# Kernel optimization log

Hardware: AMD Instinct MI355X
Metric: run time of the kernel (lower is better)

Reference implementation:

```python
import jax, jax.numpy as jnp
import numpy as np

B = 4096
UNITS = 2048
INP = 2048


def setup_inputs() -> dict:
    key = jax.random.key(0)
    k1, k2, k3, k4 = jax.random.split(key, 4)
    pre_layer = jax.random.normal(k1, (2, B, UNITS), dtype=jnp.float32)
    x = jax.random.normal(k2, (B, INP), dtype=jnp.float32)
    W = jax.random.normal(k3, (4, UNITS, INP), dtype=jnp.float32) * 0.02
    U = jax.random.normal(k4, (4, UNITS, UNITS), dtype=jnp.float32) * 0.02
    return {"pre_layer": pre_layer, "x": x, "W": W, "U": U}


def reference(pre_layer, x, W, U):
    pre_h, pre_c = pre_layer[0], pre_layer[1]
    # Fuse the 8 matmuls into 2 batched GEMMs: gates[g] = x @ W[g].T + pre_h @ U[g].T
    gates = jnp.einsum('bi,gui->gbu', x, W) + jnp.einsum('bh,guh->gbu', pre_h, U)
    i_t = jax.nn.sigmoid(gates[0])
    f_t = jax.nn.sigmoid(gates[1])
    o_t = jax.nn.sigmoid(gates[2])
    n_c_t = jnp.tanh(gates[3])
    c = f_t * pre_c + i_t * n_c_t
    h = o_t * jnp.tanh(c)
    return jnp.stack([h, c])
```

## Files before the change

kernel.cpp:

```cpp
#include <hip/hip_runtime.h>
#include <hip/hip_bf16.h>

#define B_DIM 4096
#define UNITS_DIM 2048
#define K_DIM 4096
#define M_DIM 8192

typedef __bf16 bf16x8 __attribute__((ext_vector_type(8)));
typedef float f32x4 __attribute__((ext_vector_type(4)));

#define AS1C(p) ((const __attribute__((address_space(1))) void*)(p))
#define AS3(p)  ((__attribute__((address_space(3))) void*)(p))

__device__ __forceinline__ float fast_sigmoid(float x) {
    return 1.0f / (1.0f + __expf(-x));
}
__device__ __forceinline__ float fast_tanh(float x) {
    return 2.0f / (1.0f + __expf(-2.0f * x)) - 1.0f;
}

__global__ void convert_act(const float* __restrict__ pre_h,
                            const float* __restrict__ x,
                            __hip_bfloat16* __restrict__ Abf) {
    const long long idx = (long long)blockIdx.x * blockDim.x + threadIdx.x;
    const long long e = idx * 8;
    const int b = (int)(e >> 12);
    const int k = (int)(e & 4095);
    const float* src = (k < UNITS_DIM)
        ? (x + (long long)b * UNITS_DIM + k)
        : (pre_h + (long long)b * UNITS_DIM + (k - UNITS_DIM));
    float4 f0 = ((const float4*)src)[0];
    float4 f1 = ((const float4*)src)[1];
    union { __hip_bfloat16 h[8]; uint4 u4; } p;
    p.h[0] = __float2bfloat16(f0.x); p.h[1] = __float2bfloat16(f0.y);
    p.h[2] = __float2bfloat16(f0.z); p.h[3] = __float2bfloat16(f0.w);
    p.h[4] = __float2bfloat16(f1.x); p.h[5] = __float2bfloat16(f1.y);
    p.h[6] = __float2bfloat16(f1.z); p.h[7] = __float2bfloat16(f1.w);
    *(uint4*)(Abf + e) = p.u4;
}

__global__ void convert_wu(const float* __restrict__ W,
                           const float* __restrict__ U,
                           __hip_bfloat16* __restrict__ Bbf) {
    const long long idx = (long long)blockIdx.x * blockDim.x + threadIdx.x;
    const long long e = idx * 8;
    const int n = (int)(e >> 12);
    const int k = (int)(e & 4095);
    const int u = n >> 2;
    const int g = n & 3;
    const float* src = (k < UNITS_DIM)
        ? (W + ((long long)g * UNITS_DIM + u) * UNITS_DIM + k)
        : (U + ((long long)g * UNITS_DIM + u) * UNITS_DIM + (k - UNITS_DIM));
    float4 f0 = ((const float4*)src)[0];
    float4 f1 = ((const float4*)src)[1];
    union { __hip_bfloat16 h[8]; uint4 u4; } p;
    p.h[0] = __float2bfloat16(f0.x); p.h[1] = __float2bfloat16(f0.y);
    p.h[2] = __float2bfloat16(f0.z); p.h[3] = __float2bfloat16(f0.w);
    p.h[4] = __float2bfloat16(f1.x); p.h[5] = __float2bfloat16(f1.y);
    p.h[6] = __float2bfloat16(f1.z); p.h[7] = __float2bfloat16(f1.w);
    *(uint4*)(Bbf + e) = p.u4;
}

__global__ __launch_bounds__(512, 2) void lstm_gemm(
    const __hip_bfloat16* __restrict__ Wc,
    const __hip_bfloat16* __restrict__ Ac,
    const float* __restrict__ pre_c,
    float* __restrict__ out)
{
    __shared__ __hip_bfloat16 As[4 * 8192];
    __shared__ __hip_bfloat16 Bs[4 * 8192];

    const int tid  = threadIdx.x;
    const int lane = tid & 63;
    const int wave = tid >> 6;

    const int bid  = blockIdx.x;
    const int wgid = (bid & 7) * 64 + (bid >> 3);
    const int m_base = (wgid & 31) * 256;
    const int n_base = (wgid >> 5) * 256;

    const int wm  = (wave >> 2) * 128;
    const int wn  = (wave & 3) * 64;
    const int l15 = lane & 15;
    const int lq  = lane >> 4;
    const int keyr = (l15 >> 1) & 3;

    const int aofs = (wm + l15) * 32 + ((lq ^ keyr) * 8);
    const int bofs = (wn + l15) * 32 + ((lq ^ keyr) * 8);

    const int r0 = tid >> 2;
    const int gc = (((tid & 3) ^ ((tid >> 3) & 3)) * 8);
    const __hip_bfloat16* wg0 = Wc + (size_t)(m_base + r0) * K_DIM + gc;
    const __hip_bfloat16* ag0 = Ac + (size_t)(n_base + r0) * K_DIM + gc;

#define STAGE(T) do {                                                          \
        const int sb_ = (T) & 3;                                               \
        const size_t ko_ = (size_t)(T) * 32;                                   \
        __builtin_amdgcn_global_load_lds(AS1C(wg0 + ko_),                      \
            AS3(As + sb_ * 8192 + tid * 8), 16, 0, 0);                         \
        __builtin_amdgcn_global_load_lds(AS1C(wg0 + (size_t)128 * K_DIM + ko_),\
            AS3(As + sb_ * 8192 + 4096 + tid * 8), 16, 0, 0);                  \
        __builtin_amdgcn_global_load_lds(AS1C(ag0 + ko_),                      \
            AS3(Bs + sb_ * 8192 + tid * 8), 16, 0, 0);                         \
        __builtin_amdgcn_global_load_lds(AS1C(ag0 + (size_t)128 * K_DIM + ko_),\
            AS3(Bs + sb_ * 8192 + 4096 + tid * 8), 16, 0, 0);                  \
    } while (0)

    f32x4 acc[8][4] = {};

    STAGE(0);
    STAGE(1);
    STAGE(2);
    asm volatile("s_waitcnt vmcnt(8)" ::: "memory");
    __builtin_amdgcn_s_barrier();

    for (int t = 0; t < 128; ++t) {
        const int buf = t & 3;
        const __hip_bfloat16* Ab = As + buf * 8192 + aofs;
        const __hip_bfloat16* Bb = Bs + buf * 8192 + bofs;
        bf16x8 af[8], bfv[4];
#pragma unroll
        for (int mi = 0; mi < 8; ++mi)
            af[mi] = *(const bf16x8*)(Ab + mi * 512);
#pragma unroll
        for (int ni = 0; ni < 4; ++ni)
            bfv[ni] = *(const bf16x8*)(Bb + ni * 512);

        if (t < 125) STAGE(t + 3);

        __builtin_amdgcn_sched_barrier(0);
        asm volatile("s_waitcnt lgkmcnt(0)" ::: "memory");
        if (t < 125)
            asm volatile("s_waitcnt vmcnt(8)" ::: "memory");
        else if (t == 125)
            asm volatile("s_waitcnt vmcnt(4)" ::: "memory");
        else
            asm volatile("s_waitcnt vmcnt(0)" ::: "memory");
        __builtin_amdgcn_s_barrier();
        __builtin_amdgcn_sched_barrier(0);

        __builtin_amdgcn_s_setprio(1);
#pragma unroll
        for (int mi = 0; mi < 8; ++mi)
#pragma unroll
            for (int ni = 0; ni < 4; ++ni)
                acc[mi][ni] = __builtin_amdgcn_mfma_f32_16x16x32_bf16(
                    af[mi], bfv[ni], acc[mi][ni], 0, 0, 0);
        __builtin_amdgcn_s_setprio(0);
    }
#undef STAGE

#pragma unroll
    for (int mi = 0; mi < 8; ++mi) {
        const int u = ((m_base + wm + mi * 16) >> 2) + lq;
#pragma unroll
        for (int ni = 0; ni < 4; ++ni) {
            const int b = n_base + wn + ni * 16 + l15;
            f32x4 gv = acc[mi][ni];
            float i_t = fast_sigmoid(gv[0]);
            float f_t = fast_sigmoid(gv[1]);
            float o_t = fast_sigmoid(gv[2]);
            float n_t = fast_tanh(gv[3]);
            float pc  = pre_c[(size_t)b * UNITS_DIM + u];
            float c   = f_t * pc + i_t * n_t;
            float h   = o_t * fast_tanh(c);
            out[(size_t)b * UNITS_DIM + u] = h;
            out[(size_t)B_DIM * UNITS_DIM + (size_t)b * UNITS_DIM + u] = c;
        }
    }
}

extern "C" void kernel_launch(void* const* d_in, const int* in_sizes, int n_in,
                              void* d_out, int out_size, void* d_ws, size_t ws_size,
                              hipStream_t stream) {
    const float* pre_layer = (const float*)d_in[0];
    const float* x         = (const float*)d_in[1];
    const float* W         = (const float*)d_in[2];
    const float* U         = (const float*)d_in[3];
    float* out = (float*)d_out;

    const float* pre_h = pre_layer;
    const float* pre_c = pre_layer + (size_t)B_DIM * UNITS_DIM;

    __hip_bfloat16* Abf = (__hip_bfloat16*)d_ws;
    __hip_bfloat16* Bbf = (__hip_bfloat16*)((char*)d_ws +
                          (size_t)B_DIM * K_DIM * sizeof(__hip_bfloat16));

    convert_act<<<8192, 256, 0, stream>>>(pre_h, x, Abf);
    convert_wu<<<16384, 256, 0, stream>>>(W, U, Bbf);

    lstm_gemm<<<512, 512, 0, stream>>>(Bbf, Abf, pre_c, out);
}
```

Measured before the change: 505.2 us.

## Restructure GEMM main loop into four-phase ping-pong schedule with split stages

Replaces the 4-deep single-phase k-loop with a double-buffered 64-wide k-step split into four sub-phases. Each phase loads half the A fragments, issues one A or B half-stage of global-to-LDS loads, then runs 16 MFMAs between barriers. The aim is to interleave LDS reads, global prefetch and MFMA work more finely and reduce register pressure for fragments. In exchange it adds more barriers per k-step and a tighter vmcnt accounting that must match the issue order.

Measured after the change: 642.4 us. +27.2%, slower.

```diff
diff --git a/kernel.cpp b/kernel.cpp
--- a/kernel.cpp
+++ b/kernel.cpp
@@ -67,8 +67,8 @@
     const float* __restrict__ pre_c,
     float* __restrict__ out)
 {
-    __shared__ __hip_bfloat16 As[4 * 8192];
-    __shared__ __hip_bfloat16 Bs[4 * 8192];
+    __shared__ __hip_bfloat16 As[32768];
+    __shared__ __hip_bfloat16 Bs[32768];
 
     const int tid  = threadIdx.x;
     const int lane = tid & 63;
@@ -83,72 +83,122 @@
     const int wn  = (wave & 3) * 64;
     const int l15 = lane & 15;
     const int lq  = lane >> 4;
-    const int keyr = (l15 >> 1) & 3;
-
-    const int aofs = (wm + l15) * 32 + ((lq ^ keyr) * 8);
-    const int bofs = (wn + l15) * 32 + ((lq ^ keyr) * 8);
-
-    const int r0 = tid >> 2;
+    const int key = (l15 >> 1) & 3;
+
+    const int aro = (wm + l15) * 32 + ((lq ^ key) * 8);
+    const int bro = (wn + l15) * 32 + ((lq ^ key) * 8);
+
     const int gc = (((tid & 3) ^ ((tid >> 3) & 3)) * 8);
-    const __hip_bfloat16* wg0 = Wc + (size_t)(m_base + r0) * K_DIM + gc;
-    const __hip_bfloat16* ag0 = Ac + (size_t)(n_base + r0) * K_DIM + gc;
-
-#define STAGE(T) do {                                                          \
-        const int sb_ = (T) & 3;                                               \
-        const size_t ko_ = (size_t)(T) * 32;                                   \
+    const __hip_bfloat16* wg0 = Wc + (size_t)(m_base + (tid >> 2)) * K_DIM + gc;
+    const __hip_bfloat16* ag0 = Ac + (size_t)(n_base + (tid >> 2)) * K_DIM + gc;
+
+#define STAGE_A(T, KK) do {                                                    \
+        const int b_ = ((T) & 1) * 16384 + (KK) * 8192;                        \
+        const size_t ko_ = (size_t)(T) * 64 + (KK) * 32;                       \
         __builtin_amdgcn_global_load_lds(AS1C(wg0 + ko_),                      \
-            AS3(As + sb_ * 8192 + tid * 8), 16, 0, 0);                         \
+            AS3(As + b_ + tid * 8), 16, 0, 0);                                 \
         __builtin_amdgcn_global_load_lds(AS1C(wg0 + (size_t)128 * K_DIM + ko_),\
-            AS3(As + sb_ * 8192 + 4096 + tid * 8), 16, 0, 0);                  \
+            AS3(As + b_ + 4096 + tid * 8), 16, 0, 0);                          \
+    } while (0)
+#define STAGE_B(T, KK) do {                                                    \
+        const int b_ = ((T) & 1) * 16384 + (KK) * 8192;                        \
+        const size_t ko_ = (size_t)(T) * 64 + (KK) * 32;                       \
         __builtin_amdgcn_global_load_lds(AS1C(ag0 + ko_),                      \
-            AS3(Bs + sb_ * 8192 + tid * 8), 16, 0, 0);                         \
+            AS3(Bs + b_ + tid * 8), 16, 0, 0);                                 \
         __builtin_amdgcn_global_load_lds(AS1C(ag0 + (size_t)128 * K_DIM + ko_),\
-            AS3(Bs + sb_ * 8192 + 4096 + tid * 8), 16, 0, 0);                  \
+            AS3(Bs + b_ + 4096 + tid * 8), 16, 0, 0);                          \
     } while (0)
 
+#define PHASE_SYNC() do {                                                      \
+        __builtin_amdgcn_s_barrier();                                          \
+        asm volatile("s_waitcnt lgkmcnt(0)" ::: "memory");                     \
+        __builtin_amdgcn_sched_barrier(0);                                     \
+    } while (0)
+
     f32x4 acc[8][4] = {};
 
-    STAGE(0);
-    STAGE(1);
-    STAGE(2);
-    asm volatile("s_waitcnt vmcnt(8)" ::: "memory");
+    STAGE_B(0, 0); STAGE_A(0, 0); STAGE_B(0, 1); STAGE_A(0, 1);
+    STAGE_B(1, 0); STAGE_A(1, 0); STAGE_B(1, 1);
+    asm volatile("s_waitcnt vmcnt(6)" ::: "memory");
     __builtin_amdgcn_s_barrier();
 
-    for (int t = 0; t < 128; ++t) {
-        const int buf = t & 3;
-        const __hip_bfloat16* Ab = As + buf * 8192 + aofs;
-        const __hip_bfloat16* Bb = Bs + buf * 8192 + bofs;
-        bf16x8 af[8], bfv[4];
-#pragma unroll
-        for (int mi = 0; mi < 8; ++mi)
-            af[mi] = *(const bf16x8*)(Ab + mi * 512);
+    for (int k = 0; k < 64; ++k) {
+        const int buf = (k & 1) * 16384;
+        const __hip_bfloat16* Ab = As + buf + aro;
+        const __hip_bfloat16* Bb = Bs + buf + bro;
+        bf16x8 af[4], bfv[4];
+
+#pragma unroll
+        for (int mi = 0; mi < 4; ++mi) af[mi] = *(const bf16x8*)(Ab + mi * 512);
+#pragma unroll
+        for (int ni = 0; ni < 4; ++ni) bfv[ni] = *(const bf16x8*)(Bb + ni * 512);
+        if (k <= 62) STAGE_A(k + 1, 1);
+        PHASE_SYNC();
+        __builtin_amdgcn_s_setprio(1);
+#pragma unroll
+        for (int mi = 0; mi < 4; ++mi)
+#pragma unroll
+            for (int ni = 0; ni < 4; ++ni)
+                acc[mi][ni] = __builtin_amdgcn_mfma_f32_16x16x32_bf16(
+                    af[mi], bfv[ni], acc[mi][ni], 0, 0, 0);
+        __builtin_amdgcn_s_setprio(0);
+        __builtin_amdgcn_s_barrier();
+
+#pragma unroll
+        for (int mi = 0; mi < 4; ++mi)
+            af[mi] = *(const bf16x8*)(Ab + (4 + mi) * 512);
+        if (k <= 61) STAGE_B(k + 2, 0);
+        PHASE_SYNC();
+        __builtin_amdgcn_s_setprio(1);
+#pragma unroll
+        for (int mi = 0; mi < 4; ++mi)
+#pragma unroll
+            for (int ni = 0; ni < 4; ++ni)
+                acc[4 + mi][ni] = __builtin_amdgcn_mfma_f32_16x16x32_bf16(
+                    af[mi], bfv[ni], acc[4 + mi][ni], 0, 0, 0);
+        __builtin_amdgcn_s_setprio(0);
+        __builtin_amdgcn_s_barrier();
+
+#pragma unroll
+        for (int mi = 0; mi < 4; ++mi)
+            af[mi] = *(const bf16x8*)(Ab + 8192 + mi * 512);
 #pragma unroll
         for (int ni = 0; ni < 4; ++ni)
-            bfv[ni] = *(const bf16x8*)(Bb + ni * 512);
-
-        if (t < 125) STAGE(t + 3);
-
-        __builtin_amdgcn_sched_barrier(0);
-        asm volatile("s_waitcnt lgkmcnt(0)" ::: "memory");
-        if (t < 125)
-            asm volatile("s_waitcnt vmcnt(8)" ::: "memory");
-        else if (t == 125)
-            asm volatile("s_waitcnt vmcnt(4)" ::: "memory");
+            bfv[ni] = *(const bf16x8*)(Bb + 8192 + ni * 512);
+        if (k <= 61) STAGE_A(k + 2, 0);
+        PHASE_SYNC();
+        __builtin_amdgcn_s_setprio(1);
+#pragma unroll
+        for (int mi = 0; mi < 4; ++mi)
+#pragma unroll
+            for (int ni = 0; ni < 4; ++ni)
+                acc[mi][ni] = __builtin_amdgcn_mfma_f32_16x16x32_bf16(
+                    af[mi], bfv[ni], acc[mi][ni], 0, 0, 0);
+        __builtin_amdgcn_s_setprio(0);
+        __builtin_amdgcn_s_barrier();
+
+#pragma unroll
+        for (int mi = 0; mi < 4; ++mi)
+            af[mi] = *(const bf16x8*)(Ab + 8192 + (4 + mi) * 512);
+        if (k <= 61) STAGE_B(k + 2, 1);
+        if (k <= 61)
+            asm volatile("s_waitcnt vmcnt(6)" ::: "memory");
         else
             asm volatile("s_waitcnt vmcnt(0)" ::: "memory");
-        __builtin_amdgcn_s_barrier();
-        __builtin_amdgcn_sched_barrier(0);
-
-        __builtin_amdgcn_s_setprio(1);
-#pragma unroll
-        for (int mi = 0; mi < 8; ++mi)
-#pragma unroll
-            for (int ni = 0; ni < 4; ++ni)
-                acc[mi][ni] = __builtin_amdgcn_mfma_f32_16x16x32_bf16(
-                    af[mi], bfv[ni], acc[mi][ni], 0, 0, 0);
-        __builtin_amdgcn_s_setprio(0);
+        PHASE_SYNC();
+        __builtin_amdgcn_s_setprio(1);
+#pragma unroll
+        for (int mi = 0; mi < 4; ++mi)
+#pragma unroll
+            for (int ni = 0; ni < 4; ++ni)
+                acc[4 + mi][ni] = __builtin_amdgcn_mfma_f32_16x16x32_bf16(
+                    af[mi], bfv[ni], acc[4 + mi][ni], 0, 0, 0);
+        __builtin_amdgcn_s_setprio(0);
+        __builtin_amdgcn_s_barrier();
     }
-#undef STAGE
+#undef STAGE_A
+#undef STAGE_B
+#undef PHASE_SYNC
 
 #pragma unroll
     for (int mi = 0; mi < 8; ++mi) {
```
